# Performance work log

Measured on AMD Instinct MI355X. Metric: run time of the kernel, lower is better.

## Reference

```python
import jax, jax.numpy as jnp
import numpy as np

IN_C, OUT_C, K = 32, 32, 3
PAD = 1


def setup_inputs() -> dict:
    key = jax.random.key(0)
    kx, kw, kb = jax.random.split(key, 3)
    x = jax.random.normal(kx, (16, IN_C, 256, 256), dtype=jnp.float32)
    # Kaiming-ish init scale for the conv weight, matching nn.Conv2d defaults roughly
    fan_in = IN_C * K * K
    w = jax.random.normal(kw, (OUT_C, IN_C, K, K), dtype=jnp.float32) / np.sqrt(fan_in)
    b = jax.random.normal(kb, (OUT_C,), dtype=jnp.float32) * 0.01
    return {"x": x, "weight": w, "bias": b}


def reference(x, weight, bias):
    # Faithful math of SparseConv2d.forward: the block-sparse Triton path computes
    # the same result as a dense conv (zero blocks contribute zero), so the
    # reference is a standard 3x3 stride-1 pad-1 conv, NCHW / OIHW layout.
    y = jax.lax.conv_general_dilated(
        x, weight,
        window_strides=(1, 1),
        padding=((PAD, PAD), (PAD, PAD)),
        dimension_numbers=("NCHW", "OIHW", "NCHW"),
    )
    return y + bias[None, :, None, None]
```

## Files before the change

kernel.cpp:

```cpp
#include <hip/hip_runtime.h>


constexpr int N_  = 16;
constexpr int C_  = 32;
constexpr int OC_ = 32;
constexpr int H_  = 256;
constexpr int W_  = 256;

constexpr int XSTR = 20;
constexpr int XROW = 258 * XSTR;
constexpr int WSTRD = 36;
constexpr int WELEMS = 9 * 32 * WSTRD;
constexpr int WBYTES = WELEMS * 2;

typedef __attribute__((ext_vector_type(4)))  short short4v;
typedef __attribute__((ext_vector_type(8)))  short short8v;
typedef __attribute__((ext_vector_type(16))) float float16v;
typedef __attribute__((ext_vector_type(4)))  float floatx4;

static __device__ __forceinline__ unsigned short f2bf(float f) {
    unsigned int u = __float_as_uint(f);
    unsigned int r = (u + 0x7FFFu + ((u >> 16) & 1u)) >> 16;
    return (unsigned short)r;
}

static __device__ __forceinline__ unsigned cvtpk(float lo, float hi) {
    unsigned r;
    asm("v_cvt_pk_bf16_f32 %0, %1, %2" : "=v"(r) : "v"(lo), "v"(hi));
    return r;
}

static __device__ __forceinline__ short8v load8(const unsigned short* p) {
    short4v lo = *(const short4v*)p;
    short4v hi = *(const short4v*)(p + 4);
    return __builtin_shufflevector(lo, hi, 0, 1, 2, 3, 4, 5, 6, 7);
}

static __device__ __forceinline__ void bar_lgkm() {
    asm volatile("s_waitcnt lgkmcnt(0)" ::: "memory");
    __builtin_amdgcn_s_barrier();
}

__global__ void conv_w_prep(const float* __restrict__ wgt,
                            unsigned short* __restrict__ wp) {
    const int i = blockIdx.x * 256 + threadIdx.x;
    if (i >= OC_ * C_ * 9) return;
    const float v = wgt[i];
    const int oc  = i / 288;
    const int rem = i - oc * 288;
    const int ic  = rem / 9;
    const int t9  = rem - ic * 9;
    wp[(t9 * 32 + oc) * WSTRD + ic] = f2bf(v);
}

template<bool USE_WS>
__global__ __launch_bounds__(512, 4) void conv3x3_mfma_kernel(
    const float* __restrict__ x,
    const float* __restrict__ wgt,
    const float* __restrict__ bias,
    const unsigned short* __restrict__ wpk,
    float* __restrict__ out)
{
    __shared__ __align__(16) unsigned short ldsX[4 * XROW];
    __shared__ __align__(16) unsigned short ldsW[WELEMS];

    const int tid = threadIdx.x;

    const int id = blockIdx.x;
    const int L  = (id & 7) * 256 + (id >> 3);
    const int n  = L >> 7;
    const int h  = (L & 127) * 2;

    const int lane = tid & 63;
    const int wv   = tid >> 6;
    const int rsel = wv >> 2;
    const int col  = lane & 31;
    const int qd   = lane >> 5;
    const int w0a  = (wv & 3) * 64;
    const int w0b  = (wv & 3) * 64 + 32;

    const int r4  = tid >> 7;
    const int t7  = tid & 127;
    const int wlo = t7 & 31;
    const int icq = t7 >> 5;
    const size_t HW = (size_t)H_ * W_;

    float2 a0[4], a1[4], b0r[4], b1r[4];
    auto load_half = [&](int half) {
        const int icg0 = half * 16 + 2 * icq;
        const int icg1 = half * 16 + 2 * (icq + 4);
        const int hy = h - 1 + r4;
        if (hy >= 0 && hy < H_) {
            const float* pA0 = x + ((size_t)(n * C_ + icg0) * H_ + hy) * W_;
            const float* pA1 = pA0 + HW;
            const float* pB0 = x + ((size_t)(n * C_ + icg1) * H_ + hy) * W_;
            const float* pB1 = pB0 + HW;
            #pragma unroll
            for (int wb = 0; wb < 4; ++wb) {
                const int w = wb * 64 + 2 * wlo;
                a0[wb]  = *(const float2*)(pA0 + w);
                a1[wb]  = *(const float2*)(pA1 + w);
                b0r[wb] = *(const float2*)(pB0 + w);
                b1r[wb] = *(const float2*)(pB1 + w);
            }
        } else {
            #pragma unroll
            for (int wb = 0; wb < 4; ++wb) {
                a0[wb] = a1[wb] = b0r[wb] = b1r[wb] = make_float2(0.f, 0.f);
            }
        }
    };
    load_half(0);

    if (USE_WS) {
        const int4* src = (const int4*)wpk;
        int4* dstW = (int4*)&ldsW[0];
        #pragma unroll
        for (int i2 = 0; i2 < 3; ++i2) {
            const int idx = tid + i2 * 512;
            if (idx < WBYTES / 16) dstW[idx] = src[idx];
        }
    } else {
        for (int i = tid; i < OC_ * C_ * 9; i += 512) {
            const float v = wgt[i];
            const int oc  = i / 288;
            const int rem = i - oc * 288;
            const int ic  = rem / 9;
            const int t9  = rem - ic * 9;
            ldsW[(t9 * 32 + oc) * WSTRD + ic] = f2bf(v);
        }
    }

    float16v acc0, acc1;
    #pragma unroll
    for (int r = 0; r < 16; ++r) {
        const float bv = bias[(r & 3) + 8 * (r >> 2) + 4 * qd];
        acc0[r] = bv;
        acc1[r] = bv;
    }

    auto write_half = [&]() {
        unsigned short* dst = &ldsX[r4 * XROW];
        #pragma unroll
        for (int wb = 0; wb < 4; ++wb) {
            const int w = wb * 64 + 2 * wlo;
            *(unsigned*)&dst[(w + 1) * XSTR + 2 * icq]       = cvtpk(a0[wb].x,  a1[wb].x);
            *(unsigned*)&dst[(w + 2) * XSTR + 2 * icq]       = cvtpk(a0[wb].y,  a1[wb].y);
            *(unsigned*)&dst[(w + 1) * XSTR + 2 * (icq + 4)] = cvtpk(b0r[wb].x, b1r[wb].x);
            *(unsigned*)&dst[(w + 2) * XSTR + 2 * (icq + 4)] = cvtpk(b0r[wb].y, b1r[wb].y);
        }
    };

    auto mfma_half = [&](int half) {
        #pragma unroll
        for (int kh = 0; kh < 3; ++kh) {
            #pragma unroll
            for (int kw = 0; kw < 3; ++kw) {
                const int t9 = kh * 3 + kw;
                const short8v av =
                    load8(&ldsW[(t9 * 32 + col) * WSTRD + half * 16 + qd * 8]);
                const short8v bf0 =
                    load8(&ldsX[(rsel + kh) * XROW + (w0a + col + kw) * XSTR + qd * 8]);
                const short8v bf1 =
                    load8(&ldsX[(rsel + kh) * XROW + (w0b + col + kw) * XSTR + qd * 8]);
                acc0 = __builtin_amdgcn_mfma_f32_32x32x16_bf16(av, bf0, acc0, 0, 0, 0);
                acc1 = __builtin_amdgcn_mfma_f32_32x32x16_bf16(av, bf1, acc1, 0, 0, 0);
            }
        }
    };

    write_half();
    if (tid < 32) {
        const int r  = tid >> 3;
        const int q  = tid & 7;
        const int wi = (q & 4) ? 257 : 0;
        const int c  = q & 3;
        *(unsigned long long*)&ldsX[r * XROW + wi * XSTR + c * 4] = 0ull;
    }
    bar_lgkm();

    load_half(1);
    mfma_half(0);
    bar_lgkm();

    write_half();
    bar_lgkm();
    mfma_half(1);

    bar_lgkm();
    float* scr = (float*)&ldsX[0];
    #pragma unroll
    for (int rr = 0; rr < 2; ++rr) {
        if (rsel == rr) {
            #pragma unroll
            for (int r = 0; r < 16; ++r) {
                const int oc = (r & 3) + 8 * (r >> 2) + 4 * qd;
                scr[oc * 256 + w0a + col] = acc0[r];
                scr[oc * 256 + w0b + col] = acc1[r];
            }
        }
        bar_lgkm();
        float* outp = out + (size_t)n * OC_ * HW + (size_t)(h + rr) * W_;
        #pragma unroll
        for (int k = 0; k < 4; ++k) {
            const int oc = wv * 4 + k;
            const floatx4 v = *(const floatx4*)&scr[oc * 256 + lane * 4];
            floatx4* dp = (floatx4*)(outp + (size_t)oc * HW + lane * 4);
            __builtin_nontemporal_store(v, dp);
        }
        if (rr == 0) bar_lgkm();
    }
}

extern "C" void kernel_launch(void* const* d_in, const int* in_sizes, int n_in,
                              void* d_out, int out_size, void* d_ws, size_t ws_size,
                              hipStream_t stream) {
    const float* x    = (const float*)d_in[0];
    const float* wgt  = (const float*)d_in[1];
    const float* bias = (const float*)d_in[2];
    float* out        = (float*)d_out;

    dim3 grid(N_ * H_ / 2);
    dim3 block(512);

    if (d_ws != nullptr && ws_size >= (size_t)WBYTES) {
        unsigned short* wp = (unsigned short*)d_ws;
        conv_w_prep<<<dim3(36), dim3(256), 0, stream>>>(wgt, wp);
        conv3x3_mfma_kernel<true><<<grid, block, 0, stream>>>(x, wgt, bias, wp, out);
    } else {
        conv3x3_mfma_kernel<false><<<grid, block, 0, stream>>>(x, wgt, bias, nullptr, out);
    }
}
```

Baseline: 242.2 us.

## Keep weight fragments in registers, drop weight LDS, issue all input loads upfront

Weights are pre-packed in MFMA A-fragment order and each lane loads its 18 bf16x8 fragments straight into registers, so the weight LDS buffer and its per-tile reads go away. Both channel halves of the input tile are now loaded from global memory at kernel start instead of the second half overlapping the first MFMA pass. Launch bounds rise to 6 blocks per CU to use the freed LDS. The cost is a large jump in register use (72 VGPRs of weights plus 64 floats of staged input), which may clash with the higher occupancy target and cause spills.

```diff
diff --git a/kernel.cpp b/kernel.cpp
--- a/kernel.cpp
+++ b/kernel.cpp
@@ -6,23 +6,18 @@
 constexpr int OC_ = 32;
 constexpr int H_  = 256;
 constexpr int W_  = 256;
+constexpr int HW_ = H_ * W_;
 
 constexpr int XSTR = 20;
 constexpr int XROW = 258 * XSTR;
-constexpr int WSTRD = 36;
-constexpr int WELEMS = 9 * 32 * WSTRD;
-constexpr int WBYTES = WELEMS * 2;
+constexpr int WGROUPS = 9 * 2 * 2 * 32;
+constexpr int WBYTES  = WGROUPS * 16;
 
 typedef __attribute__((ext_vector_type(4)))  short short4v;
 typedef __attribute__((ext_vector_type(8)))  short short8v;
+typedef __attribute__((ext_vector_type(4)))  int   int4v;
 typedef __attribute__((ext_vector_type(16))) float float16v;
 typedef __attribute__((ext_vector_type(4)))  float floatx4;
-
-static __device__ __forceinline__ unsigned short f2bf(float f) {
-    unsigned int u = __float_as_uint(f);
-    unsigned int r = (u + 0x7FFFu + ((u >> 16) & 1u)) >> 16;
-    return (unsigned short)r;
-}
 
 static __device__ __forceinline__ unsigned cvtpk(float lo, float hi) {
     unsigned r;
@@ -42,27 +37,33 @@
 }
 
 __global__ void conv_w_prep(const float* __restrict__ wgt,
-                            unsigned short* __restrict__ wp) {
-    const int i = blockIdx.x * 256 + threadIdx.x;
-    if (i >= OC_ * C_ * 9) return;
-    const float v = wgt[i];
-    const int oc  = i / 288;
-    const int rem = i - oc * 288;
-    const int ic  = rem / 9;
-    const int t9  = rem - ic * 9;
-    wp[(t9 * 32 + oc) * WSTRD + ic] = f2bf(v);
+                            unsigned* __restrict__ wp) {
+    const int g = blockIdx.x * 256 + threadIdx.x;
+    if (g >= WGROUPS) return;
+    const int oc  = g & 31;
+    const int q   = g >> 5;
+    const int qd  = q & 1;
+    const int hf  = (q >> 1) & 1;
+    const int t9  = q >> 2;
+    const int icb = hf * 16 + qd * 8;
+    float v[8];
+    #pragma unroll
+    for (int j = 0; j < 8; ++j) v[j] = wgt[(oc * 32 + icb + j) * 9 + t9];
+    wp[g * 4 + 0] = cvtpk(v[0], v[1]);
+    wp[g * 4 + 1] = cvtpk(v[2], v[3]);
+    wp[g * 4 + 2] = cvtpk(v[4], v[5]);
+    wp[g * 4 + 3] = cvtpk(v[6], v[7]);
 }
 
 template<bool USE_WS>
-__global__ __launch_bounds__(512, 4) void conv3x3_mfma_kernel(
+__global__ __launch_bounds__(512, 6) void conv3x3_mfma_kernel(
     const float* __restrict__ x,
     const float* __restrict__ wgt,
     const float* __restrict__ bias,
-    const unsigned short* __restrict__ wpk,
+    const unsigned* __restrict__ wpk,
     float* __restrict__ out)
 {
     __shared__ __align__(16) unsigned short ldsX[4 * XROW];
-    __shared__ __align__(16) unsigned short ldsW[WELEMS];
 
     const int tid = threadIdx.x;
 
@@ -83,51 +84,71 @@
     const int t7  = tid & 127;
     const int wlo = t7 & 31;
     const int icq = t7 >> 5;
-    const size_t HW = (size_t)H_ * W_;
-
-    float2 a0[4], a1[4], b0r[4], b1r[4];
-    auto load_half = [&](int half) {
-        const int icg0 = half * 16 + 2 * icq;
-        const int icg1 = half * 16 + 2 * (icq + 4);
+    const size_t HW = (size_t)HW_;
+
+    float2 A0[4], A1[4], B0[4], B1[4];
+    float2 C0[4], C1[4], D0[4], D1[4];
+    {
         const int hy = h - 1 + r4;
         if (hy >= 0 && hy < H_) {
-            const float* pA0 = x + ((size_t)(n * C_ + icg0) * H_ + hy) * W_;
-            const float* pA1 = pA0 + HW;
-            const float* pB0 = x + ((size_t)(n * C_ + icg1) * H_ + hy) * W_;
-            const float* pB1 = pB0 + HW;
+            #pragma unroll
+            for (int hf = 0; hf < 2; ++hf) {
+                const int icg0 = hf * 16 + 2 * icq;
+                const int icg1 = hf * 16 + 2 * (icq + 4);
+                const float* pA0 = x + ((size_t)(n * C_ + icg0) * H_ + hy) * W_;
+                const float* pA1 = pA0 + HW;
+                const float* pB0 = x + ((size_t)(n * C_ + icg1) * H_ + hy) * W_;
+                const float* pB1 = pB0 + HW;
+                #pragma unroll
+                for (int wb = 0; wb < 4; ++wb) {
+                    const int w = wb * 64 + 2 * wlo;
+                    if (hf == 0) {
+                        A0[wb] = *(const float2*)(pA0 + w);
+                        A1[wb] = *(const float2*)(pA1 + w);
+                        B0[wb] = *(const float2*)(pB0 + w);
+                        B1[wb] = *(const float2*)(pB1 + w);
+                    } else {
+                        C0[wb] = *(const float2*)(pA0 + w);
+                        C1[wb] = *(const float2*)(pA1 + w);
+                        D0[wb] = *(const float2*)(pB0 + w);
+                        D1[wb] = *(const float2*)(pB1 + w);
+                    }
+                }
+            }
+        } else {
             #pragma unroll
             for (int wb = 0; wb < 4; ++wb) {
-                const int w = wb * 64 + 2 * wlo;
-                a0[wb]  = *(const float2*)(pA0 + w);
-                a1[wb]  = *(const float2*)(pA1 + w);
-                b0r[wb] = *(const float2*)(pB0 + w);
-                b1r[wb] = *(const float2*)(pB1 + w);
-            }
-        } else {
-            #pragma unroll
-            for (int wb = 0; wb < 4; ++wb) {
-                a0[wb] = a1[wb] = b0r[wb] = b1r[wb] = make_float2(0.f, 0.f);
-            }
-        }
-    };
-    load_half(0);
-
+                A0[wb] = A1[wb] = B0[wb] = B1[wb] = make_float2(0.f, 0.f);
+                C0[wb] = C1[wb] = D0[wb] = D1[wb] = make_float2(0.f, 0.f);
+            }
+        }
+    }
+
+    short8v af[18];
     if (USE_WS) {
-        const int4* src = (const int4*)wpk;
-        int4* dstW = (int4*)&ldsW[0];
-        #pragma unroll
-        for (int i2 = 0; i2 < 3; ++i2) {
-            const int idx = tid + i2 * 512;
-            if (idx < WBYTES / 16) dstW[idx] = src[idx];
+        #pragma unroll
+        for (int t9 = 0; t9 < 9; ++t9) {
+            #pragma unroll
+            for (int hf = 0; hf < 2; ++hf) {
+                const int g = ((t9 * 2 + hf) * 2 + qd) * 32 + col;
+                af[t9 * 2 + hf] = __builtin_bit_cast(short8v,
+                                      *(const int4v*)(wpk + (size_t)g * 4));
+            }
         }
     } else {
-        for (int i = tid; i < OC_ * C_ * 9; i += 512) {
-            const float v = wgt[i];
-            const int oc  = i / 288;
-            const int rem = i - oc * 288;
-            const int ic  = rem / 9;
-            const int t9  = rem - ic * 9;
-            ldsW[(t9 * 32 + oc) * WSTRD + ic] = f2bf(v);
+        #pragma unroll
+        for (int t9 = 0; t9 < 9; ++t9) {
+            #pragma unroll
+            for (int hf = 0; hf < 2; ++hf) {
+                const int icb = hf * 16 + qd * 8;
+                unsigned u[4];
+                #pragma unroll
+                for (int jj = 0; jj < 4; ++jj)
+                    u[jj] = cvtpk(wgt[(col * 32 + icb + 2 * jj) * 9 + t9],
+                                  wgt[(col * 32 + icb + 2 * jj + 1) * 9 + t9]);
+                int4v iv; iv.x = u[0]; iv.y = u[1]; iv.z = u[2]; iv.w = u[3];
+                af[t9 * 2 + hf] = __builtin_bit_cast(short8v, iv);
+            }
         }
     }
 
@@ -139,37 +160,36 @@
         acc1[r] = bv;
     }
 
-    auto write_half = [&]() {
+    auto write_half = [&](float2 (&P0)[4], float2 (&P1)[4],
+                          float2 (&Q0)[4], float2 (&Q1)[4]) {
         unsigned short* dst = &ldsX[r4 * XROW];
         #pragma unroll
         for (int wb = 0; wb < 4; ++wb) {
             const int w = wb * 64 + 2 * wlo;
-            *(unsigned*)&dst[(w + 1) * XSTR + 2 * icq]       = cvtpk(a0[wb].x,  a1[wb].x);
-            *(unsigned*)&dst[(w + 2) * XSTR + 2 * icq]       = cvtpk(a0[wb].y,  a1[wb].y);
-            *(unsigned*)&dst[(w + 1) * XSTR + 2 * (icq + 4)] = cvtpk(b0r[wb].x, b1r[wb].x);
-            *(unsigned*)&dst[(w + 2) * XSTR + 2 * (icq + 4)] = cvtpk(b0r[wb].y, b1r[wb].y);
+            *(unsigned*)&dst[(w + 1) * XSTR + 2 * icq]       = cvtpk(P0[wb].x, P1[wb].x);
+            *(unsigned*)&dst[(w + 2) * XSTR + 2 * icq]       = cvtpk(P0[wb].y, P1[wb].y);
+            *(unsigned*)&dst[(w + 1) * XSTR + 2 * (icq + 4)] = cvtpk(Q0[wb].x, Q1[wb].x);
+            *(unsigned*)&dst[(w + 2) * XSTR + 2 * (icq + 4)] = cvtpk(Q0[wb].y, Q1[wb].y);
         }
     };
 
-    auto mfma_half = [&](int half) {
+    auto mfma_half = [&](int hf) {
         #pragma unroll
         for (int kh = 0; kh < 3; ++kh) {
             #pragma unroll
             for (int kw = 0; kw < 3; ++kw) {
                 const int t9 = kh * 3 + kw;
-                const short8v av =
-                    load8(&ldsW[(t9 * 32 + col) * WSTRD + half * 16 + qd * 8]);
                 const short8v bf0 =
                     load8(&ldsX[(rsel + kh) * XROW + (w0a + col + kw) * XSTR + qd * 8]);
                 const short8v bf1 =
                     load8(&ldsX[(rsel + kh) * XROW + (w0b + col + kw) * XSTR + qd * 8]);
-                acc0 = __builtin_amdgcn_mfma_f32_32x32x16_bf16(av, bf0, acc0, 0, 0, 0);
-                acc1 = __builtin_amdgcn_mfma_f32_32x32x16_bf16(av, bf1, acc1, 0, 0, 0);
+                acc0 = __builtin_amdgcn_mfma_f32_32x32x16_bf16(af[t9 * 2 + hf], bf0, acc0, 0, 0, 0);
+                acc1 = __builtin_amdgcn_mfma_f32_32x32x16_bf16(af[t9 * 2 + hf], bf1, acc1, 0, 0, 0);
             }
         }
     };
 
-    write_half();
+    write_half(A0, A1, B0, B1);
     if (tid < 32) {
         const int r  = tid >> 3;
         const int q  = tid & 7;
@@ -179,11 +199,10 @@
     }
     bar_lgkm();
 
-    load_half(1);
     mfma_half(0);
     bar_lgkm();
 
-    write_half();
+    write_half(C0, C1, D0, D1);
     bar_lgkm();
     mfma_half(1);
 
@@ -224,8 +243,8 @@
     dim3 block(512);
 
     if (d_ws != nullptr && ws_size >= (size_t)WBYTES) {
-        unsigned short* wp = (unsigned short*)d_ws;
-        conv_w_prep<<<dim3(36), dim3(256), 0, stream>>>(wgt, wp);
+        unsigned* wp = (unsigned*)d_ws;
+        conv_w_prep<<<dim3(5), dim3(256), 0, stream>>>(wgt, wp);
         conv3x3_mfma_kernel<true><<<grid, block, 0, stream>>>(x, wgt, bias, wp, out);
     } else {
         conv3x3_mfma_kernel<false><<<grid, block, 0, stream>>>(x, wgt, bias, nullptr, out);
```

Result: slower. 357.4 us (+47.5%).
